# Performance work log

Measured on AMD Instinct MI355X. Metric: run time of the kernel, lower is better.

Reference implementation:

```python
import jax, jax.numpy as jnp
import numpy as np

NUM, K = 5, 3  # grid intervals and spline order, as in KANLayer(num=5, k=3)

def _grid(num=NUM, k=K, lo=-1.0, hi=1.0):
    # base grid: num+1 points on [lo,hi], extended by k knots on each side (pykan extend_grid)
    h = (hi - lo) / num
    return jnp.linspace(lo - k * h, hi + k * h, num + 1 + 2 * k, dtype=jnp.float32)

def b_spline_basis(x, grid, k=K):
    # Cox-de Boor recursion, identical to pykan B_batch. x: (B, In) -> (B, In, num+k)
    xe = x[..., None]
    b = ((xe >= grid[:-1]) & (xe < grid[1:])).astype(x.dtype)  # order-0 indicators
    for d in range(1, k + 1):
        left = (xe - grid[:-(d + 1)]) / (grid[d:-1] - grid[:-(d + 1)])
        right = (grid[d + 1:] - xe) / (grid[d + 1:] - grid[1:-d])
        b = left * b[..., :-1] + right * b[..., 1:]
    return b

def kan_layer(x, coef, sb, ssp, grid):
    # x: (B, In); coef: (Out, In, nb); sb/ssp: (Out, In). mask == 1.
    basis = b_spline_basis(x, grid)                       # (B, In, nb)
    spline = jnp.einsum('big,oig->boi', basis, coef)      # per-edge spline value
    y = sb[None] * jax.nn.silu(x)[:, None, :] + ssp[None] * spline  # (B, Out, In)
    return y.sum(axis=2)                                  # (B, Out)

def setup_inputs() -> dict:
    key = jax.random.key(0)
    ks = jax.random.split(key, 3)
    B, IN, H, OUT, NB = 128, 3072, 256, 10, NUM + K
    return {
        "x": jax.random.normal(ks[0], (B, IN), jnp.float32),
        "coef1": 0.1 * jax.random.normal(ks[1], (H, IN, NB), jnp.float32),
        "scale_base1": jnp.ones((H, IN), jnp.float32),
        "scale_sp1": jnp.ones((H, IN), jnp.float32),
        "coef2": 0.1 * jax.random.normal(ks[2], (OUT, H, NB), jnp.float32),
        "scale_base2": jnp.ones((OUT, H), jnp.float32),
        "scale_sp2": jnp.ones((OUT, H), jnp.float32),
    }

def reference(x, coef1, scale_base1, scale_sp1, coef2, scale_base2, scale_sp2):
    g = _grid()
    h = kan_layer(x, coef1, scale_base1, scale_sp1, g)
    h = jax.nn.selu(h)
    return kan_layer(h, coef2, scale_base2, scale_sp2, g)
```

## Files before the change

kernel.cpp:

```cpp
#include <hip/hip_runtime.h>
#include <hip/hip_bf16.h>
#include <math.h>


#define B_DIM   128
#define IN1     3072
#define OUT1    256
#define NB      8
#define OUT2    10

#define KTOT    27648
#define ROWB    55296
#define SPLITK  108
#define BN      64

typedef short  bf16x8 __attribute__((ext_vector_type(8)));
typedef float  f32x4  __attribute__((ext_vector_type(4)));
typedef unsigned short ushort_t;
typedef unsigned int u32;

__device__ __forceinline__ ushort_t f2bf(float f) {
    union { __hip_bfloat16 h; ushort_t u; } v;
    v.h = __float2bfloat16(f);
    return v.u;
}
__device__ __forceinline__ float bf2f(ushort_t h) {
    union { float f; u32 u; } v; v.u = ((u32)h) << 16;
    return v.f;
}

__device__ __forceinline__ void gl_lds16(const void* g, void* l) {
    __builtin_amdgcn_global_load_lds(
        (const __attribute__((address_space(1))) u32*)g,
        (__attribute__((address_space(3))) u32*)l, 16, 0, 0);
}

__device__ __forceinline__ void basis_silu(float x, float w[8], float& sil) {
    sil = x / (1.0f + __expf(-x));
    float u  = (x + 2.2f) * 2.5f;
    float uf = floorf(u);
    int   j  = (int)uf;
    float t  = u - uf;
    float omt = 1.0f - t;
    float t2 = t * t, t3 = t2 * t;
    float w0 = omt * omt * omt * (1.0f / 6.0f);
    float w1 = (3.0f * t3 - 6.0f * t2 + 4.0f) * (1.0f / 6.0f);
    float w2 = (-3.0f * t3 + 3.0f * t2 + 3.0f * t + 1.0f) * (1.0f / 6.0f);
    float w3 = t3 * (1.0f / 6.0f);
    bool valid = (u >= 0.0f) && (u < 11.0f);
#pragma unroll
    for (int g = 0; g < 8; ++g) {
        int m = g - j + 3;
        float v = (m == 0) ? w0 : (m == 1) ? w1 : (m == 2) ? w2 : (m == 3) ? w3 : 0.0f;
        w[g] = valid ? v : 0.0f;
    }
}

__device__ __forceinline__ float selu_f(float x) {
    const float scale = 1.0507009873554805f;
    const float alpha = 1.6732632423543772f;
    return (x > 0.0f) ? scale * x : scale * alpha * (__expf(x) - 1.0f);
}

__global__ __launch_bounds__(128) void kconv_a(const float* __restrict__ x,
                                               char* __restrict__ Ag) {
    const int gid = blockIdx.x * 128 + threadIdx.x;
    const int b  = gid / 384;
    const int ig = gid - b * 384;
    const int i0 = ig * 8;

    float4 x0 = *reinterpret_cast<const float4*>(x + (size_t)b * IN1 + i0);
    float4 x1 = *reinterpret_cast<const float4*>(x + (size_t)b * IN1 + i0 + 4);
    float xa[8] = {x0.x, x0.y, x0.z, x0.w, x1.x, x1.y, x1.z, x1.w};

    float bs[8][8], sil[8];
#pragma unroll
    for (int p = 0; p < 8; ++p) basis_silu(xa[p], bs[p], sil[p]);

    char* rowp = Ag + (size_t)b * ROWB;
    const int qsw = ((ig & 7) ^ (b & 7)) << 4;
#pragma unroll
    for (int s = 0; s < 9; ++s) {
        ushort_t v[8];
#pragma unroll
        for (int p = 0; p < 8; ++p)
            v[p] = f2bf((s < 8) ? bs[p][s] : sil[p]);
        *reinterpret_cast<uint4*>(rowp + (s * 48 + (ig >> 3)) * 128 + qsw) =
            *reinterpret_cast<const uint4*>(v);
    }
}

__global__ __launch_bounds__(128) void kconv_w(const float* __restrict__ coef1,
                                               const float* __restrict__ sb1,
                                               const float* __restrict__ ssp1,
                                               char* __restrict__ Wg) {
    const int gid = blockIdx.x * 128 + threadIdx.x;
    const int o  = gid / 384;
    const int ig = gid - o * 384;
    const int i0 = ig * 8;

    float cf[8][8], sspv[8], sbv[8];
#pragma unroll
    for (int p = 0; p < 8; ++p) {
        const float* cp = coef1 + ((size_t)o * IN1 + i0 + p) * NB;
        float4 c0 = *reinterpret_cast<const float4*>(cp);
        float4 c1 = *reinterpret_cast<const float4*>(cp + 4);
        cf[p][0] = c0.x; cf[p][1] = c0.y; cf[p][2] = c0.z; cf[p][3] = c0.w;
        cf[p][4] = c1.x; cf[p][5] = c1.y; cf[p][6] = c1.z; cf[p][7] = c1.w;
    }
    {
        float4 s0 = *reinterpret_cast<const float4*>(ssp1 + (size_t)o * IN1 + i0);
        float4 s1 = *reinterpret_cast<const float4*>(ssp1 + (size_t)o * IN1 + i0 + 4);
        sspv[0]=s0.x; sspv[1]=s0.y; sspv[2]=s0.z; sspv[3]=s0.w;
        sspv[4]=s1.x; sspv[5]=s1.y; sspv[6]=s1.z; sspv[7]=s1.w;
        float4 b0 = *reinterpret_cast<const float4*>(sb1 + (size_t)o * IN1 + i0);
        float4 b1 = *reinterpret_cast<const float4*>(sb1 + (size_t)o * IN1 + i0 + 4);
        sbv[0]=b0.x; sbv[1]=b0.y; sbv[2]=b0.z; sbv[3]=b0.w;
        sbv[4]=b1.x; sbv[5]=b1.y; sbv[6]=b1.z; sbv[7]=b1.w;
    }

    char* rowp = Wg + (size_t)o * ROWB;
    const int qsw = ((ig & 7) ^ (o & 7)) << 4;
#pragma unroll
    for (int s = 0; s < 9; ++s) {
        ushort_t v[8];
#pragma unroll
        for (int p = 0; p < 8; ++p)
            v[p] = f2bf((s < 8) ? cf[p][s] * sspv[p] : sbv[p]);
        *reinterpret_cast<uint4*>(rowp + (s * 48 + (ig >> 3)) * 128 + qsw) =
            *reinterpret_cast<const uint4*>(v);
    }
}

__global__ __launch_bounds__(512) void kgemm(const char* __restrict__ Ag,
                                             const char* __restrict__ Wg,
                                             ushort_t* __restrict__ partial) {
    __shared__ __align__(16) char lds[2][24576];

    const int tid = threadIdx.x;
    const int w   = tid >> 6, l = tid & 63;
    const int nt  = blockIdx.x, kc = blockIdx.y;
    const int o0  = nt * BN;

    const int ar0 = tid >> 3;
    const int ar1 = 64 + (tid >> 3);
    const int aq  = tid & 7;
    const char* Asrc0 = Ag + (size_t)ar0 * ROWB + ((aq ^ (ar0 & 7)) << 4);
    const char* Asrc1 = Ag + (size_t)ar1 * ROWB + ((aq ^ (ar1 & 7)) << 4);
    const int wr = tid >> 3;
    const char* Wsrc = Wg + (size_t)(o0 + wr) * ROWB + ((aq ^ (wr & 7)) << 4);

#define ISSUE(ss, buf)                                                        \
    {                                                                         \
        const int cb = (kc * 4 + (ss)) * 128;                                 \
        char* base = &lds[buf][0];                                            \
        gl_lds16(Asrc0 + cb, base + w * 1024);                                \
        gl_lds16(Asrc1 + cb, base + 8192 + w * 1024);                         \
        gl_lds16(Wsrc  + cb, base + 16384 + w * 1024);                        \
    }

    f32x4 acc[2][2];
#pragma unroll
    for (int a = 0; a < 2; ++a)
#pragma unroll
        for (int bq = 0; bq < 2; ++bq) acc[a][bq] = (f32x4){0.f, 0.f, 0.f, 0.f};

    const int mq = w >> 1, nq = w & 1;
    const int r16 = l & 15, k16 = l >> 4;

    ISSUE(0, 0)
    ISSUE(1, 1)

#pragma unroll
    for (int s = 0; s < 4; ++s) {
        if (s < 3) { asm volatile("s_waitcnt vmcnt(3)" ::: "memory"); }
        else       { asm volatile("s_waitcnt vmcnt(0)" ::: "memory"); }
        __builtin_amdgcn_s_barrier();
        asm volatile("" ::: "memory");

        const char* Ab = &lds[s & 1][0];
        const char* Wb = &lds[s & 1][16384];
#pragma unroll
        for (int ks = 0; ks < 2; ++ks) {
            const int qf = ks * 4 + k16;
            bf16x8 bf[2], af[2];
#pragma unroll
            for (int bq = 0; bq < 2; ++bq) {
                const int rn = nq * 32 + bq * 16 + r16;
                bf[bq] = *reinterpret_cast<const bf16x8*>(Wb + rn * 128 + ((qf ^ (rn & 7)) << 4));
            }
#pragma unroll
            for (int a = 0; a < 2; ++a) {
                const int rm = mq * 32 + a * 16 + r16;
                af[a] = *reinterpret_cast<const bf16x8*>(Ab + rm * 128 + ((qf ^ (rm & 7)) << 4));
            }
#pragma unroll
            for (int a = 0; a < 2; ++a)
#pragma unroll
                for (int bq = 0; bq < 2; ++bq)
                    acc[a][bq] = __builtin_amdgcn_mfma_f32_16x16x32_bf16(af[a], bf[bq], acc[a][bq], 0, 0, 0);
        }

        __builtin_amdgcn_s_barrier();
        asm volatile("" ::: "memory");
        if (s == 0) ISSUE(2, 0)
        if (s == 1) ISSUE(3, 1)
    }
#undef ISSUE

    ushort_t* pp = partial + (size_t)kc * (B_DIM * OUT1);
#pragma unroll
    for (int a = 0; a < 2; ++a) {
#pragma unroll
        for (int bq = 0; bq < 2; ++bq) {
            const int col = o0 + nq * 32 + bq * 16 + r16;
#pragma unroll
            for (int r = 0; r < 4; ++r) {
                const int row = mq * 32 + a * 16 + k16 * 4 + r;
                pp[(size_t)row * OUT1 + col] = f2bf(acc[a][bq][r]);
            }
        }
    }
}

#define CPG (SPLITK / 4)

__global__ __launch_bounds__(1024) void kreduce(const ushort_t* __restrict__ partial,
                                                const float* __restrict__ coef2,
                                                const float* __restrict__ sb2,
                                                const float* __restrict__ ssp2,
                                                float* __restrict__ out) {
    const int b = blockIdx.x;
    const int t = threadIdx.x;
    const int o = t & 255;
    const int g = t >> 8;
    const ushort_t* pp = partial + ((size_t)g * CPG * B_DIM + b) * OUT1 + o;
    float sum = 0.0f;
#pragma unroll
    for (int c = 0; c < CPG; ++c)
        sum += bf2f(pp[(size_t)c * (B_DIM * OUT1)]);

    __shared__ float hred[4][OUT1];
    hred[g][o] = sum;
    __syncthreads();
    const float hv = hred[0][o] + hred[1][o] + hred[2][o] + hred[3][o];

    const float sh = selu_f(hv);
    float w8[8], sil;
    basis_silu(sh, w8, sil);

    float accs[OUT2];
#pragma unroll
    for (int oo = 0; oo < OUT2; ++oo) {
        const float* cp = coef2 + ((size_t)oo * OUT1 + o) * NB;
        float4 c0 = *reinterpret_cast<const float4*>(cp);
        float4 c1 = *reinterpret_cast<const float4*>(cp + 4);
        float dot = w8[0] * c0.x + w8[1] * c0.y + w8[2] * c0.z + w8[3] * c0.w +
                    w8[4] * c1.x + w8[5] * c1.y + w8[6] * c1.z + w8[7] * c1.w;
        accs[oo] = sb2[oo * OUT1 + o] * sil + ssp2[oo * OUT1 + o] * dot;
    }

    __shared__ float red[16][OUT2];
    const int lane = t & 63, wv = t >> 6;
#pragma unroll
    for (int oo = 0; oo < OUT2; ++oo) {
        float v = accs[oo];
#pragma unroll
        for (int off = 32; off >= 1; off >>= 1) v += __shfl_xor(v, off, 64);
        if (lane == 0) red[wv][oo] = v;
    }
    __syncthreads();
    if (t < OUT2)
        out[b * OUT2 + t] = red[0][t] + red[1][t] + red[2][t] + red[3][t];
}

extern "C" void kernel_launch(void* const* d_in, const int* in_sizes, int n_in,
                              void* d_out, int out_size, void* d_ws, size_t ws_size,
                              hipStream_t stream) {
    const float* x     = (const float*)d_in[0];
    const float* coef1 = (const float*)d_in[1];
    const float* sb1   = (const float*)d_in[2];
    const float* ssp1  = (const float*)d_in[3];
    const float* coef2 = (const float*)d_in[4];
    const float* sb2   = (const float*)d_in[5];
    const float* ssp2  = (const float*)d_in[6];
    float* out = (float*)d_out;

    char*     Ag      = (char*)d_ws;
    char*     Wg      = Ag + (size_t)B_DIM * ROWB;
    ushort_t* partial = (ushort_t*)(Wg + (size_t)OUT1 * ROWB);

    kconv_a<<<384, 128, 0, stream>>>(x, Ag);
    kconv_w<<<768, 128, 0, stream>>>(coef1, sb1, ssp1, Wg);
    kgemm<<<dim3(OUT1 / BN, SPLITK), 512, 0, stream>>>(Ag, Wg, partial);
    kreduce<<<B_DIM, 1024, 0, stream>>>(partial, coef2, sb2, ssp2, out);
}
```

Measured before the change: 44.82 us.

## Merge conversion kernels and replace split-K partial buffer with atomic accumulation

```diff
diff --git a/kernel.cpp b/kernel.cpp
--- a/kernel.cpp
+++ b/kernel.cpp
@@ -23,10 +23,6 @@
     union { __hip_bfloat16 h; ushort_t u; } v;
     v.h = __float2bfloat16(f);
     return v.u;
-}
-__device__ __forceinline__ float bf2f(ushort_t h) {
-    union { float f; u32 u; } v; v.u = ((u32)h) << 16;
-    return v.f;
 }
 
 __device__ __forceinline__ void gl_lds16(const void* g, void* l) {
@@ -62,79 +58,84 @@
     return (x > 0.0f) ? scale * x : scale * alpha * (__expf(x) - 1.0f);
 }
 
-__global__ __launch_bounds__(128) void kconv_a(const float* __restrict__ x,
-                                               char* __restrict__ Ag) {
-    const int gid = blockIdx.x * 128 + threadIdx.x;
-    const int b  = gid / 384;
-    const int ig = gid - b * 384;
-    const int i0 = ig * 8;
-
-    float4 x0 = *reinterpret_cast<const float4*>(x + (size_t)b * IN1 + i0);
-    float4 x1 = *reinterpret_cast<const float4*>(x + (size_t)b * IN1 + i0 + 4);
-    float xa[8] = {x0.x, x0.y, x0.z, x0.w, x1.x, x1.y, x1.z, x1.w};
-
-    float bs[8][8], sil[8];
-#pragma unroll
-    for (int p = 0; p < 8; ++p) basis_silu(xa[p], bs[p], sil[p]);
-
-    char* rowp = Ag + (size_t)b * ROWB;
-    const int qsw = ((ig & 7) ^ (b & 7)) << 4;
-#pragma unroll
-    for (int s = 0; s < 9; ++s) {
-        ushort_t v[8];
-#pragma unroll
-        for (int p = 0; p < 8; ++p)
-            v[p] = f2bf((s < 8) ? bs[p][s] : sil[p]);
-        *reinterpret_cast<uint4*>(rowp + (s * 48 + (ig >> 3)) * 128 + qsw) =
-            *reinterpret_cast<const uint4*>(v);
-    }
-}
-
-__global__ __launch_bounds__(128) void kconv_w(const float* __restrict__ coef1,
-                                               const float* __restrict__ sb1,
-                                               const float* __restrict__ ssp1,
-                                               char* __restrict__ Wg) {
-    const int gid = blockIdx.x * 128 + threadIdx.x;
-    const int o  = gid / 384;
-    const int ig = gid - o * 384;
-    const int i0 = ig * 8;
-
-    float cf[8][8], sspv[8], sbv[8];
-#pragma unroll
-    for (int p = 0; p < 8; ++p) {
-        const float* cp = coef1 + ((size_t)o * IN1 + i0 + p) * NB;
-        float4 c0 = *reinterpret_cast<const float4*>(cp);
-        float4 c1 = *reinterpret_cast<const float4*>(cp + 4);
-        cf[p][0] = c0.x; cf[p][1] = c0.y; cf[p][2] = c0.z; cf[p][3] = c0.w;
-        cf[p][4] = c1.x; cf[p][5] = c1.y; cf[p][6] = c1.z; cf[p][7] = c1.w;
-    }
-    {
-        float4 s0 = *reinterpret_cast<const float4*>(ssp1 + (size_t)o * IN1 + i0);
-        float4 s1 = *reinterpret_cast<const float4*>(ssp1 + (size_t)o * IN1 + i0 + 4);
-        sspv[0]=s0.x; sspv[1]=s0.y; sspv[2]=s0.z; sspv[3]=s0.w;
-        sspv[4]=s1.x; sspv[5]=s1.y; sspv[6]=s1.z; sspv[7]=s1.w;
-        float4 b0 = *reinterpret_cast<const float4*>(sb1 + (size_t)o * IN1 + i0);
-        float4 b1 = *reinterpret_cast<const float4*>(sb1 + (size_t)o * IN1 + i0 + 4);
-        sbv[0]=b0.x; sbv[1]=b0.y; sbv[2]=b0.z; sbv[3]=b0.w;
-        sbv[4]=b1.x; sbv[5]=b1.y; sbv[6]=b1.z; sbv[7]=b1.w;
-    }
-
-    char* rowp = Wg + (size_t)o * ROWB;
-    const int qsw = ((ig & 7) ^ (o & 7)) << 4;
-#pragma unroll
-    for (int s = 0; s < 9; ++s) {
-        ushort_t v[8];
-#pragma unroll
-        for (int p = 0; p < 8; ++p)
-            v[p] = f2bf((s < 8) ? cf[p][s] * sspv[p] : sbv[p]);
-        *reinterpret_cast<uint4*>(rowp + (s * 48 + (ig >> 3)) * 128 + qsw) =
-            *reinterpret_cast<const uint4*>(v);
+__global__ __launch_bounds__(128) void kconv(const float* __restrict__ x,
+                                             const float* __restrict__ coef1,
+                                             const float* __restrict__ sb1,
+                                             const float* __restrict__ ssp1,
+                                             char* __restrict__ Ag,
+                                             char* __restrict__ Wg,
+                                             float* __restrict__ h) {
+    const int blk = blockIdx.x;
+    if (blk < 384) {
+        if (blk < 256) h[blk * 128 + threadIdx.x] = 0.0f;
+
+        const int gid = blk * 128 + threadIdx.x;
+        const int b  = gid / 384;
+        const int ig = gid - b * 384;
+        const int i0 = ig * 8;
+
+        float4 x0 = *reinterpret_cast<const float4*>(x + (size_t)b * IN1 + i0);
+        float4 x1 = *reinterpret_cast<const float4*>(x + (size_t)b * IN1 + i0 + 4);
+        float xa[8] = {x0.x, x0.y, x0.z, x0.w, x1.x, x1.y, x1.z, x1.w};
+
+        float bs[8][8], sil[8];
+#pragma unroll
+        for (int p = 0; p < 8; ++p) basis_silu(xa[p], bs[p], sil[p]);
+
+        char* rowp = Ag + (size_t)b * ROWB;
+        const int qsw = ((ig & 7) ^ (b & 7)) << 4;
+#pragma unroll
+        for (int s = 0; s < 9; ++s) {
+            ushort_t v[8];
+#pragma unroll
+            for (int p = 0; p < 8; ++p)
+                v[p] = f2bf((s < 8) ? bs[p][s] : sil[p]);
+            *reinterpret_cast<uint4*>(rowp + (s * 48 + (ig >> 3)) * 128 + qsw) =
+                *reinterpret_cast<const uint4*>(v);
+        }
+    } else {
+        const int gid = (blk - 384) * 128 + threadIdx.x;
+        const int o  = gid / 384;
+        const int ig = gid - o * 384;
+        const int i0 = ig * 8;
+
+        float cf[8][8], sspv[8], sbv[8];
+#pragma unroll
+        for (int p = 0; p < 8; ++p) {
+            const float* cp = coef1 + ((size_t)o * IN1 + i0 + p) * NB;
+            float4 c0 = *reinterpret_cast<const float4*>(cp);
+            float4 c1 = *reinterpret_cast<const float4*>(cp + 4);
+            cf[p][0] = c0.x; cf[p][1] = c0.y; cf[p][2] = c0.z; cf[p][3] = c0.w;
+            cf[p][4] = c1.x; cf[p][5] = c1.y; cf[p][6] = c1.z; cf[p][7] = c1.w;
+        }
+        {
+            float4 s0 = *reinterpret_cast<const float4*>(ssp1 + (size_t)o * IN1 + i0);
+            float4 s1 = *reinterpret_cast<const float4*>(ssp1 + (size_t)o * IN1 + i0 + 4);
+            sspv[0]=s0.x; sspv[1]=s0.y; sspv[2]=s0.z; sspv[3]=s0.w;
+            sspv[4]=s1.x; sspv[5]=s1.y; sspv[6]=s1.z; sspv[7]=s1.w;
+            float4 b0 = *reinterpret_cast<const float4*>(sb1 + (size_t)o * IN1 + i0);
+            float4 b1 = *reinterpret_cast<const float4*>(sb1 + (size_t)o * IN1 + i0 + 4);
+            sbv[0]=b0.x; sbv[1]=b0.y; sbv[2]=b0.z; sbv[3]=b0.w;
+            sbv[4]=b1.x; sbv[5]=b1.y; sbv[6]=b1.z; sbv[7]=b1.w;
+        }
+
+        char* rowp = Wg + (size_t)o * ROWB;
+        const int qsw = ((ig & 7) ^ (o & 7)) << 4;
+#pragma unroll
+        for (int s = 0; s < 9; ++s) {
+            ushort_t v[8];
+#pragma unroll
+            for (int p = 0; p < 8; ++p)
+                v[p] = f2bf((s < 8) ? cf[p][s] * sspv[p] : sbv[p]);
+            *reinterpret_cast<uint4*>(rowp + (s * 48 + (ig >> 3)) * 128 + qsw) =
+                *reinterpret_cast<const uint4*>(v);
+        }
     }
 }
 
 __global__ __launch_bounds__(512) void kgemm(const char* __restrict__ Ag,
                                              const char* __restrict__ Wg,
-                                             ushort_t* __restrict__ partial) {
+                                             float* __restrict__ h) {
     __shared__ __align__(16) char lds[2][24576];
 
     const int tid = threadIdx.x;
@@ -208,7 +209,6 @@
     }
 #undef ISSUE
 
-    ushort_t* pp = partial + (size_t)kc * (B_DIM * OUT1);
 #pragma unroll
     for (int a = 0; a < 2; ++a) {
 #pragma unroll
@@ -217,34 +217,20 @@
 #pragma unroll
             for (int r = 0; r < 4; ++r) {
                 const int row = mq * 32 + a * 16 + k16 * 4 + r;
-                pp[(size_t)row * OUT1 + col] = f2bf(acc[a][bq][r]);
+                atomicAdd(&h[(size_t)row * OUT1 + col], acc[a][bq][r]);
             }
         }
     }
 }
 
-#define CPG (SPLITK / 4)
-
-__global__ __launch_bounds__(1024) void kreduce(const ushort_t* __restrict__ partial,
-                                                const float* __restrict__ coef2,
-                                                const float* __restrict__ sb2,
-                                                const float* __restrict__ ssp2,
-                                                float* __restrict__ out) {
+__global__ __launch_bounds__(256) void klayer2(const float* __restrict__ h,
+                                               const float* __restrict__ coef2,
+                                               const float* __restrict__ sb2,
+                                               const float* __restrict__ ssp2,
+                                               float* __restrict__ out) {
     const int b = blockIdx.x;
     const int t = threadIdx.x;
-    const int o = t & 255;
-    const int g = t >> 8;
-    const ushort_t* pp = partial + ((size_t)g * CPG * B_DIM + b) * OUT1 + o;
-    float sum = 0.0f;
-#pragma unroll
-    for (int c = 0; c < CPG; ++c)
-        sum += bf2f(pp[(size_t)c * (B_DIM * OUT1)]);
-
-    __shared__ float hred[4][OUT1];
-    hred[g][o] = sum;
-    __syncthreads();
-    const float hv = hred[0][o] + hred[1][o] + hred[2][o] + hred[3][o];
-
+    const float hv = h[b * OUT1 + t];
     const float sh = selu_f(hv);
     float w8[8], sil;
     basis_silu(sh, w8, sil);
@@ -252,15 +238,15 @@
     float accs[OUT2];
 #pragma unroll
     for (int oo = 0; oo < OUT2; ++oo) {
-        const float* cp = coef2 + ((size_t)oo * OUT1 + o) * NB;
+        const float* cp = coef2 + ((size_t)oo * OUT1 + t) * NB;
         float4 c0 = *reinterpret_cast<const float4*>(cp);
         float4 c1 = *reinterpret_cast<const float4*>(cp + 4);
         float dot = w8[0] * c0.x + w8[1] * c0.y + w8[2] * c0.z + w8[3] * c0.w +
                     w8[4] * c1.x + w8[5] * c1.y + w8[6] * c1.z + w8[7] * c1.w;
-        accs[oo] = sb2[oo * OUT1 + o] * sil + ssp2[oo * OUT1 + o] * dot;
-    }
-
-    __shared__ float red[16][OUT2];
+        accs[oo] = sb2[oo * OUT1 + t] * sil + ssp2[oo * OUT1 + t] * dot;
+    }
+
+    __shared__ float red[4][OUT2];
     const int lane = t & 63, wv = t >> 6;
 #pragma unroll
     for (int oo = 0; oo < OUT2; ++oo) {
@@ -286,12 +272,11 @@
     const float* ssp2  = (const float*)d_in[6];
     float* out = (float*)d_out;
 
-    char*     Ag      = (char*)d_ws;
-    char*     Wg      = Ag + (size_t)B_DIM * ROWB;
-    ushort_t* partial = (ushort_t*)(Wg + (size_t)OUT1 * ROWB);
-
-    kconv_a<<<384, 128, 0, stream>>>(x, Ag);
-    kconv_w<<<768, 128, 0, stream>>>(coef1, sb1, ssp1, Wg);
-    kgemm<<<dim3(OUT1 / BN, SPLITK), 512, 0, stream>>>(Ag, Wg, partial);
-    kreduce<<<B_DIM, 1024, 0, stream>>>(partial, coef2, sb2, ssp2, out);
-}
+    char*  Ag = (char*)d_ws;
+    char*  Wg = Ag + (size_t)B_DIM * ROWB;
+    float* h  = (float*)(Wg + (size_t)OUT1 * ROWB);
+
+    kconv<<<1152, 128, 0, stream>>>(x, coef1, sb1, ssp1, Ag, Wg, h);
+    kgemm<<<dim3(OUT1 / BN, SPLITK), 512, 0, stream>>>(Ag, Wg, h);
+    klayer2<<<B_DIM, 256, 0, stream>>>(h, coef2, sb2, ssp2, out);
+}
```

Result: faster. 43.21 us (-3.6%).
